# Kernel tuning notes

Hardware: AMD Instinct MI355X
Metric: run time of the kernel (lower is better)

The kernel has to match this reference:

```python
import jax, jax.numpy as jnp
import numpy as np

EPS = 1e-5
NEG_SLOPE = 0.01  # nn.LeakyReLU default


def _bn(x, gamma, beta, mean, var):
    # eval-mode batchnorm over last (channel) axis
    return (x - mean) * (gamma * jax.lax.rsqrt(var + EPS)) + beta


def setup_inputs() -> dict:
    key = jax.random.key(0)
    ks = jax.random.split(key, 12)
    B, N, F = 4, 256, 128
    Cin = 2 * F + 2  # edge channels (2) + pairwise concat (2F)
    inp = {
        "node_feat": jax.random.normal(ks[0], (B, N, F), jnp.float32),
        "edge_feat": jax.random.normal(ks[1], (B, N, N, 2), jnp.float32),
        # conv1: 1x1, (2F+2) -> F, no bias
        "w1": jax.random.normal(ks[2], (F, Cin), jnp.float32) * (1.0 / np.sqrt(Cin)),
        "bn1_gamma": jnp.ones((F,), jnp.float32),
        "bn1_beta": jnp.zeros((F,), jnp.float32),
        "bn1_mean": jnp.zeros((F,), jnp.float32),
        "bn1_var": jnp.ones((F,), jnp.float32),
        # conv2: 1x1, F -> F, no bias
        "w2": jax.random.normal(ks[3], (F, F), jnp.float32) * (1.0 / np.sqrt(F)),
        "bn2_gamma": jnp.ones((F,), jnp.float32),
        "bn2_beta": jnp.zeros((F,), jnp.float32),
        "bn2_mean": jnp.zeros((F,), jnp.float32),
        "bn2_var": jnp.ones((F,), jnp.float32),
        # pair_network: Linear(F, 2)
        "pw": jax.random.normal(ks[4], (2, F), jnp.float32) * (1.0 / np.sqrt(F)),
        "pb": jax.random.uniform(ks[5], (2,), jnp.float32, -0.1, 0.1),
    }
    return inp


def reference(node_feat, edge_feat, w1, bn1_gamma, bn1_beta, bn1_mean, bn1_var,
              w2, bn2_gamma, bn2_beta, bn2_mean, bn2_var, pw, pb):
    # node_feat: [B,N,F], edge_feat: [B,N,N,2]
    F = node_feat.shape[-1]
    # concat order along channels: [edge (2), P_left (F), P_right (F)]
    w_e = w1[:, :2]            # [F, 2]
    w_l = w1[:, 2:2 + F]       # [F, F]
    w_r = w1[:, 2 + F:]        # [F, F]
    # Fused broadcast-GEMM: conv1x1 over concat == sum of partial projections.
    hl = jnp.einsum('bif,gf->big', node_feat, w_l)   # [B,N,F] (row/left term)
    hr = jnp.einsum('bjf,gf->bjg', node_feat, w_r)   # [B,N,F] (col/right term)
    he = jnp.einsum('bijc,gc->bijg', edge_feat, w_e)  # [B,N,N,F]
    h = he + hl[:, :, None, :] + hr[:, None, :, :]    # [B,N,N,F]
    h = _bn(h, bn1_gamma, bn1_beta, bn1_mean, bn1_var)
    h = jnp.where(h >= 0, h, NEG_SLOPE * h)           # LeakyReLU
    # Dropout is identity in eval mode.
    h = jnp.einsum('bijf,gf->bijg', h, w2)            # conv2 1x1
    h = _bn(h, bn2_gamma, bn2_beta, bn2_mean, bn2_var)
    out = jnp.einsum('bijf,of->bijo', h, pw) + pb     # [B,N,N,2]
    return out
```

## Files before the change

kernel.cpp:

```cpp
#include <hip/hip_runtime.h>

#define EPS    1e-5f
#define NSLOPE 0.01f
#define B 4
#define N 256
#define F 128

#define WS_WE0 0
#define WS_WE1 128
#define WS_PF0 256
#define WS_PF1 384
#define WS_C   512
#define WS_S1  520
#define WS_T1  648
#define WS_HL  1024
#define WS_HR  (1024 + B*N*F)

__global__ __launch_bounds__(128) void prep0(
    const float* __restrict__ w1,
    const float* __restrict__ g1, const float* __restrict__ b1,
    const float* __restrict__ m1, const float* __restrict__ v1,
    const float* __restrict__ w2,
    const float* __restrict__ g2, const float* __restrict__ b2,
    const float* __restrict__ m2, const float* __restrict__ v2,
    const float* __restrict__ pw, const float* __restrict__ pb,
    float* __restrict__ ws) {
  __shared__ float s2s[F], t2s[F];
  int g = threadIdx.x;
  float s1v = g1[g] / sqrtf(v1[g] + EPS);
  ws[WS_S1 + g] = s1v;
  ws[WS_T1 + g] = b1[g] - m1[g] * s1v;
  ws[WS_WE0 + g] = w1[g * 258 + 0] * s1v;
  ws[WS_WE1 + g] = w1[g * 258 + 1] * s1v;
  float s2v = g2[g] / sqrtf(v2[g] + EPS);
  s2s[g] = s2v;
  t2s[g] = b2[g] - m2[g] * s2v;
  __syncthreads();
  float a0 = 0.f, a1 = 0.f;
  for (int f = 0; f < F; ++f) {
    float wv = w2[f * F + g];
    a0 = fmaf(pw[f]     * s2s[f], wv, a0);
    a1 = fmaf(pw[F + f] * s2s[f], wv, a1);
  }
  ws[WS_PF0 + g] = a0;
  ws[WS_PF1 + g] = a1;
  if (g < 2) {
    float c = pb[g];
    for (int f = 0; f < F; ++f) c += pw[g * F + f] * t2s[f];
    ws[WS_C + g] = c;
  }
}

__global__ __launch_bounds__(128) void prep1(
    const float* __restrict__ node, const float* __restrict__ w1,
    float* __restrict__ ws) {
  __shared__ float ns[8][F];
  int tid = threadIdx.x;
  int r0 = blockIdx.x * 8;
  {
    int r = tid >> 4, c = (tid & 15) * 8;
    const float* src = node + (size_t)(r0 + r) * F + c;
    *reinterpret_cast<float4*>(&ns[r][c])     = *reinterpret_cast<const float4*>(src);
    *reinterpret_cast<float4*>(&ns[r][c + 4]) = *reinterpret_cast<const float4*>(src + 4);
  }
  __syncthreads();
  int g = tid;
  float accl[8] = {0.f, 0.f, 0.f, 0.f, 0.f, 0.f, 0.f, 0.f};
  float accr[8] = {0.f, 0.f, 0.f, 0.f, 0.f, 0.f, 0.f, 0.f};
  for (int f = 0; f < F; ++f) {
    float wl = w1[g * 258 + 2 + f];
    float wr = w1[g * 258 + 130 + f];
    #pragma unroll
    for (int r = 0; r < 8; ++r) {
      float nv = ns[r][f];
      accl[r] = fmaf(nv, wl, accl[r]);
      accr[r] = fmaf(nv, wr, accr[r]);
    }
  }
  float s1v = ws[WS_S1 + g], t1v = ws[WS_T1 + g];
  float* hl = ws + WS_HL;
  float* hr = ws + WS_HR;
  #pragma unroll
  for (int r = 0; r < 8; ++r) {
    hl[(size_t)(r0 + r) * F + g] = fmaf(accl[r], s1v, t1v);
    hr[(size_t)(r0 + r) * F + g] = accr[r] * s1v;
  }
}

__global__ __launch_bounds__(256) void fused_main(
    const float* __restrict__ edge,
    const float* __restrict__ ws, float* __restrict__ out) {
  __shared__ float hls[16][132];
  __shared__ float hrs[16][132];
  int b = blockIdx.z, i0 = blockIdx.y * 16, j0 = blockIdx.x * 16;
  int tid = threadIdx.x;
  const float* hl = ws + WS_HL;
  const float* hr = ws + WS_HR;
  {
    int r = tid >> 4, c = (tid & 15) * 8;
    const float* sl = hl + (size_t)(b * N + i0 + r) * F + c;
    const float* sr = hr + (size_t)(b * N + j0 + r) * F + c;
    *reinterpret_cast<float4*>(&hls[r][c])     = *reinterpret_cast<const float4*>(sl);
    *reinterpret_cast<float4*>(&hls[r][c + 4]) = *reinterpret_cast<const float4*>(sl + 4);
    *reinterpret_cast<float4*>(&hrs[r][c])     = *reinterpret_cast<const float4*>(sr);
    *reinterpret_cast<float4*>(&hrs[r][c + 4]) = *reinterpret_cast<const float4*>(sr + 4);
  }
  __syncthreads();
  int ti = tid >> 4, tj = tid & 15;
  size_t eidx = ((size_t)(b * N + i0 + ti) * N + (j0 + tj)) * 2;
  float2 e = *reinterpret_cast<const float2*>(edge + eidx);
  float acc0 = 0.f, acc1 = 0.f;
  #pragma unroll 8
  for (int g = 0; g < F; g += 4) {
    float4 L  = *reinterpret_cast<const float4*>(&hls[ti][g]);
    float4 R  = *reinterpret_cast<const float4*>(&hrs[tj][g]);
    float4 W0 = *reinterpret_cast<const float4*>(ws + WS_WE0 + g);
    float4 W1 = *reinterpret_cast<const float4*>(ws + WS_WE1 + g);
    float4 P0 = *reinterpret_cast<const float4*>(ws + WS_PF0 + g);
    float4 P1 = *reinterpret_cast<const float4*>(ws + WS_PF1 + g);
    float v, a;
    v = L.x + R.x; v = fmaf(e.x, W0.x, v); v = fmaf(e.y, W1.x, v);
    a = v >= 0.f ? v : NSLOPE * v;
    acc0 = fmaf(P0.x, a, acc0); acc1 = fmaf(P1.x, a, acc1);
    v = L.y + R.y; v = fmaf(e.x, W0.y, v); v = fmaf(e.y, W1.y, v);
    a = v >= 0.f ? v : NSLOPE * v;
    acc0 = fmaf(P0.y, a, acc0); acc1 = fmaf(P1.y, a, acc1);
    v = L.z + R.z; v = fmaf(e.x, W0.z, v); v = fmaf(e.y, W1.z, v);
    a = v >= 0.f ? v : NSLOPE * v;
    acc0 = fmaf(P0.z, a, acc0); acc1 = fmaf(P1.z, a, acc1);
    v = L.w + R.w; v = fmaf(e.x, W0.w, v); v = fmaf(e.y, W1.w, v);
    a = v >= 0.f ? v : NSLOPE * v;
    acc0 = fmaf(P0.w, a, acc0); acc1 = fmaf(P1.w, a, acc1);
  }
  float2 o;
  o.x = acc0 + ws[WS_C + 0];
  o.y = acc1 + ws[WS_C + 1];
  *reinterpret_cast<float2*>(out + eidx) = o;
}

extern "C" void kernel_launch(void* const* d_in, const int* in_sizes, int n_in,
                              void* d_out, int out_size, void* d_ws, size_t ws_size,
                              hipStream_t stream) {
  const float* node = (const float*)d_in[0];
  const float* edge = (const float*)d_in[1];
  const float* w1   = (const float*)d_in[2];
  const float* g1   = (const float*)d_in[3];
  const float* b1   = (const float*)d_in[4];
  const float* m1   = (const float*)d_in[5];
  const float* v1   = (const float*)d_in[6];
  const float* w2   = (const float*)d_in[7];
  const float* g2   = (const float*)d_in[8];
  const float* b2   = (const float*)d_in[9];
  const float* m2   = (const float*)d_in[10];
  const float* v2   = (const float*)d_in[11];
  const float* pw   = (const float*)d_in[12];
  const float* pb   = (const float*)d_in[13];
  float* ws  = (float*)d_ws;
  float* out = (float*)d_out;

  prep0<<<1, 128, 0, stream>>>(w1, g1, b1, m1, v1, w2, g2, b2, m2, v2, pw, pb, ws);
  prep1<<<128, 128, 0, stream>>>(node, w1, ws);
  fused_main<<<dim3(N / 16, N / 16, B), 256, 0, stream>>>(edge, ws, out);
}
```

Baseline: 30.57 us.

## Register-block main kernel 2x2, stage weights in LDS, transpose w1 for coalesced prep

The main kernel now computes a 2x2 block of (i,j) pairs per thread over a 32x32 tile, so each LDS load of hl/hr rows is reused twice. The per-channel edge and pair weights are staged in shared memory instead of read from global, and LeakyReLU becomes fmaxf. The prep stage adds a parallel transpose of w1's left and right blocks with BN scale folded in, so prepB reads weights coalesced, and prepB uses 4 rows per block across 256 blocks. The main grid drops to 256 blocks, which may underfill the GPU's CUs and raises register pressure.

```diff
diff --git a/kernel.cpp b/kernel.cpp
--- a/kernel.cpp
+++ b/kernel.cpp
@@ -13,10 +13,12 @@
 #define WS_C   512
 #define WS_S1  520
 #define WS_T1  648
-#define WS_HL  1024
-#define WS_HR  (1024 + B*N*F)
-
-__global__ __launch_bounds__(128) void prep0(
+#define WS_WLT 2048
+#define WS_WRT (WS_WLT + F*F)
+#define WS_HL  (WS_WRT + F*F)
+#define WS_HR  (WS_HL + B*N*F)
+
+__global__ __launch_bounds__(128) void prepA(
     const float* __restrict__ w1,
     const float* __restrict__ g1, const float* __restrict__ b1,
     const float* __restrict__ m1, const float* __restrict__ v1,
@@ -25,8 +27,15 @@
     const float* __restrict__ m2, const float* __restrict__ v2,
     const float* __restrict__ pw, const float* __restrict__ pb,
     float* __restrict__ ws) {
+  int g = threadIdx.x;
+  if (blockIdx.x != 0) {
+    int f = blockIdx.x - 1;
+    float s1v = g1[g] / sqrtf(v1[g] + EPS);
+    ws[WS_WLT + f * F + g] = w1[g * 258 + 2 + f] * s1v;
+    ws[WS_WRT + f * F + g] = w1[g * 258 + 130 + f] * s1v;
+    return;
+  }
   __shared__ float s2s[F], t2s[F];
-  int g = threadIdx.x;
   float s1v = g1[g] / sqrtf(v1[g] + EPS);
   ws[WS_S1 + g] = s1v;
   ws[WS_T1 + g] = b1[g] - m1[g] * s1v;
@@ -51,91 +60,118 @@
   }
 }
 
-__global__ __launch_bounds__(128) void prep1(
-    const float* __restrict__ node, const float* __restrict__ w1,
+__global__ __launch_bounds__(128) void prepB(
+    const float* __restrict__ node, const float* __restrict__ ws_c,
     float* __restrict__ ws) {
-  __shared__ float ns[8][F];
-  int tid = threadIdx.x;
-  int r0 = blockIdx.x * 8;
+  __shared__ float ns[4][F];
+  int t = threadIdx.x;
+  int r0 = blockIdx.x * 4;
   {
-    int r = tid >> 4, c = (tid & 15) * 8;
-    const float* src = node + (size_t)(r0 + r) * F + c;
-    *reinterpret_cast<float4*>(&ns[r][c])     = *reinterpret_cast<const float4*>(src);
-    *reinterpret_cast<float4*>(&ns[r][c + 4]) = *reinterpret_cast<const float4*>(src + 4);
+    int r = t >> 5, c = (t & 31) * 4;
+    *reinterpret_cast<float4*>(&ns[r][c]) =
+        *reinterpret_cast<const float4*>(node + (size_t)(r0 + r) * F + c);
   }
   __syncthreads();
-  int g = tid;
-  float accl[8] = {0.f, 0.f, 0.f, 0.f, 0.f, 0.f, 0.f, 0.f};
-  float accr[8] = {0.f, 0.f, 0.f, 0.f, 0.f, 0.f, 0.f, 0.f};
+  int g = t;
+  const float* wlT = ws_c + WS_WLT;
+  const float* wrT = ws_c + WS_WRT;
+  float al[4] = {0.f, 0.f, 0.f, 0.f};
+  float ar[4] = {0.f, 0.f, 0.f, 0.f};
+  #pragma unroll 4
   for (int f = 0; f < F; ++f) {
-    float wl = w1[g * 258 + 2 + f];
-    float wr = w1[g * 258 + 130 + f];
+    float wl = wlT[f * F + g];
+    float wr = wrT[f * F + g];
     #pragma unroll
-    for (int r = 0; r < 8; ++r) {
+    for (int r = 0; r < 4; ++r) {
       float nv = ns[r][f];
-      accl[r] = fmaf(nv, wl, accl[r]);
-      accr[r] = fmaf(nv, wr, accr[r]);
+      al[r] = fmaf(nv, wl, al[r]);
+      ar[r] = fmaf(nv, wr, ar[r]);
     }
   }
-  float s1v = ws[WS_S1 + g], t1v = ws[WS_T1 + g];
+  float t1v = ws_c[WS_T1 + g];
   float* hl = ws + WS_HL;
   float* hr = ws + WS_HR;
   #pragma unroll
-  for (int r = 0; r < 8; ++r) {
-    hl[(size_t)(r0 + r) * F + g] = fmaf(accl[r], s1v, t1v);
-    hr[(size_t)(r0 + r) * F + g] = accr[r] * s1v;
+  for (int r = 0; r < 4; ++r) {
+    hl[(size_t)(r0 + r) * F + g] = al[r] + t1v;
+    hr[(size_t)(r0 + r) * F + g] = ar[r];
   }
 }
 
 __global__ __launch_bounds__(256) void fused_main(
     const float* __restrict__ edge,
     const float* __restrict__ ws, float* __restrict__ out) {
-  __shared__ float hls[16][132];
-  __shared__ float hrs[16][132];
-  int b = blockIdx.z, i0 = blockIdx.y * 16, j0 = blockIdx.x * 16;
-  int tid = threadIdx.x;
+  __shared__ float hls[32][132];
+  __shared__ float hrs[32][132];
+  __shared__ float wps[4][F];
+  int b = blockIdx.z, i0 = blockIdx.y * 32, j0 = blockIdx.x * 32;
+  int t = threadIdx.x;
   const float* hl = ws + WS_HL;
   const float* hr = ws + WS_HR;
   {
-    int r = tid >> 4, c = (tid & 15) * 8;
-    const float* sl = hl + (size_t)(b * N + i0 + r) * F + c;
-    const float* sr = hr + (size_t)(b * N + j0 + r) * F + c;
-    *reinterpret_cast<float4*>(&hls[r][c])     = *reinterpret_cast<const float4*>(sl);
-    *reinterpret_cast<float4*>(&hls[r][c + 4]) = *reinterpret_cast<const float4*>(sl + 4);
-    *reinterpret_cast<float4*>(&hrs[r][c])     = *reinterpret_cast<const float4*>(sr);
-    *reinterpret_cast<float4*>(&hrs[r][c + 4]) = *reinterpret_cast<const float4*>(sr + 4);
+    int r = t >> 3, cq = (t & 7) * 16;
+    const float* sl = hl + (size_t)(b * N + i0 + r) * F + cq;
+    const float* sr = hr + (size_t)(b * N + j0 + r) * F + cq;
+    #pragma unroll
+    for (int k = 0; k < 4; ++k) {
+      *reinterpret_cast<float4*>(&hls[r][cq + 4 * k]) =
+          *reinterpret_cast<const float4*>(sl + 4 * k);
+      *reinterpret_cast<float4*>(&hrs[r][cq + 4 * k]) =
+          *reinterpret_cast<const float4*>(sr + 4 * k);
+    }
+    reinterpret_cast<float2*>(&wps[0][0])[t] =
+        reinterpret_cast<const float2*>(ws)[t];
   }
   __syncthreads();
-  int ti = tid >> 4, tj = tid & 15;
-  size_t eidx = ((size_t)(b * N + i0 + ti) * N + (j0 + tj)) * 2;
-  float2 e = *reinterpret_cast<const float2*>(edge + eidx);
-  float acc0 = 0.f, acc1 = 0.f;
-  #pragma unroll 8
+  int ti = t >> 4, tj = t & 15;
+  int i1 = i0 + ti, i2 = i1 + 16, j1 = j0 + tj, j2 = j1 + 16;
+  const float2* e00p = reinterpret_cast<const float2*>(edge + ((size_t)(b * N + i1) * N + j1) * 2);
+  const float2* e01p = reinterpret_cast<const float2*>(edge + ((size_t)(b * N + i1) * N + j2) * 2);
+  const float2* e10p = reinterpret_cast<const float2*>(edge + ((size_t)(b * N + i2) * N + j1) * 2);
+  const float2* e11p = reinterpret_cast<const float2*>(edge + ((size_t)(b * N + i2) * N + j2) * 2);
+  float2 e00 = *e00p, e01 = *e01p, e10 = *e10p, e11 = *e11p;
+  float a00x = 0.f, a00y = 0.f, a01x = 0.f, a01y = 0.f;
+  float a10x = 0.f, a10y = 0.f, a11x = 0.f, a11y = 0.f;
+  #pragma unroll 4
   for (int g = 0; g < F; g += 4) {
-    float4 L  = *reinterpret_cast<const float4*>(&hls[ti][g]);
-    float4 R  = *reinterpret_cast<const float4*>(&hrs[tj][g]);
-    float4 W0 = *reinterpret_cast<const float4*>(ws + WS_WE0 + g);
-    float4 W1 = *reinterpret_cast<const float4*>(ws + WS_WE1 + g);
-    float4 P0 = *reinterpret_cast<const float4*>(ws + WS_PF0 + g);
-    float4 P1 = *reinterpret_cast<const float4*>(ws + WS_PF1 + g);
-    float v, a;
-    v = L.x + R.x; v = fmaf(e.x, W0.x, v); v = fmaf(e.y, W1.x, v);
-    a = v >= 0.f ? v : NSLOPE * v;
-    acc0 = fmaf(P0.x, a, acc0); acc1 = fmaf(P1.x, a, acc1);
-    v = L.y + R.y; v = fmaf(e.x, W0.y, v); v = fmaf(e.y, W1.y, v);
-    a = v >= 0.f ? v : NSLOPE * v;
-    acc0 = fmaf(P0.y, a, acc0); acc1 = fmaf(P1.y, a, acc1);
-    v = L.z + R.z; v = fmaf(e.x, W0.z, v); v = fmaf(e.y, W1.z, v);
-    a = v >= 0.f ? v : NSLOPE * v;
-    acc0 = fmaf(P0.z, a, acc0); acc1 = fmaf(P1.z, a, acc1);
-    v = L.w + R.w; v = fmaf(e.x, W0.w, v); v = fmaf(e.y, W1.w, v);
-    a = v >= 0.f ? v : NSLOPE * v;
-    acc0 = fmaf(P0.w, a, acc0); acc1 = fmaf(P1.w, a, acc1);
-  }
+    float4 L0 = *reinterpret_cast<const float4*>(&hls[ti][g]);
+    float4 L1 = *reinterpret_cast<const float4*>(&hls[ti + 16][g]);
+    float4 R0 = *reinterpret_cast<const float4*>(&hrs[tj][g]);
+    float4 R1 = *reinterpret_cast<const float4*>(&hrs[tj + 16][g]);
+    float4 W0 = *reinterpret_cast<const float4*>(&wps[0][g]);
+    float4 W1 = *reinterpret_cast<const float4*>(&wps[1][g]);
+    float4 P0 = *reinterpret_cast<const float4*>(&wps[2][g]);
+    float4 P1 = *reinterpret_cast<const float4*>(&wps[3][g]);
+#define DO_COMP(K)                                                             \
+    {                                                                          \
+      float w0 = W0.K, w1v = W1.K, p0 = P0.K, p1 = P1.K;                       \
+      float v;                                                                 \
+      v = L0.K + R0.K; v = fmaf(e00.x, w0, v); v = fmaf(e00.y, w1v, v);        \
+      v = fmaxf(v, NSLOPE * v);                                                \
+      a00x = fmaf(p0, v, a00x); a00y = fmaf(p1, v, a00y);                      \
+      v = L0.K + R1.K; v = fmaf(e01.x, w0, v); v = fmaf(e01.y, w1v, v);        \
+      v = fmaxf(v, NSLOPE * v);                                                \
+      a01x = fmaf(p0, v, a01x); a01y = fmaf(p1, v, a01y);                      \
+      v = L1.K + R0.K; v = fmaf(e10.x, w0, v); v = fmaf(e10.y, w1v, v);        \
+      v = fmaxf(v, NSLOPE * v);                                                \
+      a10x = fmaf(p0, v, a10x); a10y = fmaf(p1, v, a10y);                      \
+      v = L1.K + R1.K; v = fmaf(e11.x, w0, v); v = fmaf(e11.y, w1v, v);        \
+      v = fmaxf(v, NSLOPE * v);                                                \
+      a11x = fmaf(p0, v, a11x); a11y = fmaf(p1, v, a11y);                      \
+    }
+    DO_COMP(x) DO_COMP(y) DO_COMP(z) DO_COMP(w)
+#undef DO_COMP
+  }
+  float c0 = ws[WS_C + 0], c1 = ws[WS_C + 1];
   float2 o;
-  o.x = acc0 + ws[WS_C + 0];
-  o.y = acc1 + ws[WS_C + 1];
-  *reinterpret_cast<float2*>(out + eidx) = o;
+  o.x = a00x + c0; o.y = a00y + c1;
+  *reinterpret_cast<float2*>(out + ((size_t)(b * N + i1) * N + j1) * 2) = o;
+  o.x = a01x + c0; o.y = a01y + c1;
+  *reinterpret_cast<float2*>(out + ((size_t)(b * N + i1) * N + j2) * 2) = o;
+  o.x = a10x + c0; o.y = a10y + c1;
+  *reinterpret_cast<float2*>(out + ((size_t)(b * N + i2) * N + j1) * 2) = o;
+  o.x = a11x + c0; o.y = a11y + c1;
+  *reinterpret_cast<float2*>(out + ((size_t)(b * N + i2) * N + j2) * 2) = o;
 }
 
 extern "C" void kernel_launch(void* const* d_in, const int* in_sizes, int n_in,
@@ -158,7 +194,7 @@
   float* ws  = (float*)d_ws;
   float* out = (float*)d_out;
 
-  prep0<<<1, 128, 0, stream>>>(w1, g1, b1, m1, v1, w2, g2, b2, m2, v2, pw, pb, ws);
-  prep1<<<128, 128, 0, stream>>>(node, w1, ws);
-  fused_main<<<dim3(N / 16, N / 16, B), 256, 0, stream>>>(edge, ws, out);
-}
+  prepA<<<1 + F, 128, 0, stream>>>(w1, g1, b1, m1, v1, w2, g2, b2, m2, v2, pw, pb, ws);
+  prepB<<<256, 128, 0, stream>>>(node, ws, ws);
+  fused_main<<<dim3(N / 32, N / 32, B), 256, 0, stream>>>(edge, ws, out);
+}
```

After: 33.62 us. +10.0%, slower.
